# Optimization experiments

Hardware: AMD Instinct MI355X
Metric: run time of the kernel (lower is better)

The kernel has to match this reference:

```python
import jax, jax.numpy as jnp
import numpy as np
from math import sqrt

B, S, E, H = 4, 2048, 1024, 16
D = E // H  # per-head dim = 64


def setup_inputs() -> dict:
    key = jax.random.key(0)
    ks = jax.random.split(key, 11)
    f = lambda k, shape, scale=1.0: jax.random.normal(k, shape, dtype=jnp.float32) * scale
    return {
        "Q": f(ks[0], (B, S, E)),
        "K": f(ks[1], (B, S, E)),
        "V": f(ks[2], (B, S, E)),
        "Wq": f(ks[3], (E, E), 1.0 / sqrt(E)),
        "bq": f(ks[4], (E,), 0.02),
        "Wk": f(ks[5], (E, E), 1.0 / sqrt(E)),
        "bk": f(ks[6], (E,), 0.02),
        "Wv": f(ks[7], (E, E), 1.0 / sqrt(E)),
        "bv": f(ks[8], (E,), 0.02),
        "Wo": f(ks[9], (E, E), 1.0 / sqrt(E)),
        "bo": f(ks[10], (E,), 0.02),
    }


def reference(Q, K, V, Wq, bq, Wk, bk, Wv, bv, Wo, bo):
    # Linear projections (torch Linear: x @ W.T + b)
    q = Q @ Wq.T + bq  # [B,S,E]
    k = K @ Wk.T + bk
    v = V @ Wv.T + bv
    # torch.chunk along last dim into H heads == reshape [B,S,H,D]
    q = q.reshape(B, S, H, D)
    k = k.reshape(B, S, H, D)
    v = v.reshape(B, S, H, D)
    scale = 1.0 / sqrt(D)
    # batched-over-heads scaled dot-product attention
    scores = jnp.einsum("bqhd,bkhd->bhqk", q, k) * scale  # [B,H,S,S]
    attn = jax.nn.softmax(scores, axis=-1)
    out = jnp.einsum("bhqk,bkhd->bqhd", attn, v).reshape(B, S, E)
    # dropout p=0.0 -> identity
    return out @ Wo.T + bo
```

## Files before the change

kernel.cpp:

```cpp
#include <hip/hip_runtime.h>
#include <hip/hip_bf16.h>

#define B_SZ   4
#define S_LEN  2048
#define E_DIM  1024
#define H_NUM  16
#define D_DIM  64
#define M_ROWS (B_SZ * S_LEN)
#define QK_SCALE 0.1803368801111204f

typedef __attribute__((ext_vector_type(8))) __bf16 bf16x8;
typedef __attribute__((ext_vector_type(4))) float  f32x4;

__device__ __forceinline__ bf16x8 load8(const void* p) {
    return __builtin_bit_cast(bf16x8, *reinterpret_cast<const uint4*>(p));
}

#if defined(__has_builtin)
#if __has_builtin(__builtin_amdgcn_exp2f)
#define EXP2F(x) __builtin_amdgcn_exp2f(x)
#endif
#if __has_builtin(__builtin_amdgcn_global_load_lds)
#define HAVE_GLL 1
#endif
#endif
#ifndef EXP2F
#define EXP2F(x) exp2f(x)
#endif

__device__ __forceinline__ void stage16(const __hip_bfloat16* g, __hip_bfloat16* lbase, int lane) {
#ifdef HAVE_GLL
    __builtin_amdgcn_global_load_lds((const __attribute__((address_space(1))) unsigned int*)g,
                                     (__attribute__((address_space(3))) unsigned int*)lbase,
                                     16, 0, 0);
#else
    reinterpret_cast<uint4*>(lbase)[lane] = *reinterpret_cast<const uint4*>(g);
#endif
}

#define N8A (1 << 20)
#define N8W (1 << 17)
#define N8TOT (3 * N8A + 4 * N8W)

struct CvtArgs {
    const float* s[7];
    __hip_bfloat16* d[7];
};

__global__ __launch_bounds__(256) void cvt_all(CvtArgs a)
{
    const int i = blockIdx.x * 256 + threadIdx.x;
    if (i >= N8TOT) return;
    int seg, off;
    if (i < 3 * N8A) { seg = i >> 20;              off = i & (N8A - 1); }
    else             { const int j = i - 3 * N8A;
                       seg = 3 + (j >> 17);        off = j & (N8W - 1); }
    const float* s = a.s[seg];
    __hip_bfloat16* d = a.d[seg];
    const float4 x = reinterpret_cast<const float4*>(s)[off * 2];
    const float4 y = reinterpret_cast<const float4*>(s)[off * 2 + 1];
    __hip_bfloat16 o[8];
    o[0] = __float2bfloat16(x.x); o[1] = __float2bfloat16(x.y);
    o[2] = __float2bfloat16(x.z); o[3] = __float2bfloat16(x.w);
    o[4] = __float2bfloat16(y.x); o[5] = __float2bfloat16(y.y);
    o[6] = __float2bfloat16(y.z); o[7] = __float2bfloat16(y.w);
    reinterpret_cast<uint4*>(d)[off] = *reinterpret_cast<uint4*>(o);
}

__global__ __launch_bounds__(256) void cvt_f32_bf16(const float* __restrict__ s,
                                                    __hip_bfloat16* __restrict__ d,
                                                    int n8)
{
    const int i = blockIdx.x * 256 + threadIdx.x;
    if (i >= n8) return;
    const float4 a = reinterpret_cast<const float4*>(s)[i * 2];
    const float4 b = reinterpret_cast<const float4*>(s)[i * 2 + 1];
    __hip_bfloat16 o[8];
    o[0] = __float2bfloat16(a.x); o[1] = __float2bfloat16(a.y);
    o[2] = __float2bfloat16(a.z); o[3] = __float2bfloat16(a.w);
    o[4] = __float2bfloat16(b.x); o[5] = __float2bfloat16(b.y);
    o[6] = __float2bfloat16(b.z); o[7] = __float2bfloat16(b.w);
    reinterpret_cast<uint4*>(d)[i] = *reinterpret_cast<uint4*>(o);
}

struct GemmArgs {
    const __hip_bfloat16* A[3];
    const __hip_bfloat16* W[3];
    const float* bias[3];
    void* C[3];
    float scale[3];
    int mode[3];
};

__global__ __launch_bounds__(512, 4) void gemm_bt(GemmArgs g)
{
    __shared__ __attribute__((aligned(16))) char lds_raw[3 * 24576];

    const int tid = threadIdx.x;
    const int wid = tid >> 6, lane = tid & 63;
    const int quad = lane >> 4, l16 = lane & 15;
    const int wm = wid >> 2, wn = wid & 3;

    const int seg = blockIdx.x >> 8;
    int bid = blockIdx.x & 255;
    bid = (bid & 7) * 32 + (bid >> 3);
    const int bm = bid >> 2, bn = bid & 3;
    const int row0 = bm * 128, col0 = bn * 256;

    const __hip_bfloat16* A = g.A[seg];
    const __hip_bfloat16* W = g.W[seg];

    const int s_line = tid >> 3, s_gr = tid & 7;
    const int glin  = s_gr ^ (s_line & 7);
    const int s_row = (s_line << 1) + (glin >> 2);
    const int s_ks  = glin & 3;
    const __hip_bfloat16* gA = A + (size_t)(row0 + s_row) * E_DIM + s_ks * 8;
    const __hip_bfloat16* gB = W + (size_t)(col0 + s_row) * E_DIM + s_ks * 8;
    const int stA = wid << 10;

    const int rg   = (((l16 & 1) << 2) | quad) ^ ((l16 >> 1) & 7);
    const int aoff = (wm * 32 + (l16 >> 1)) * 128 + rg * 16;
    const int boff = (wn * 32 + (l16 >> 1)) * 128 + rg * 16;

    f32x4 acc[4][4];
    const f32x4 zero = {0.f, 0.f, 0.f, 0.f};
#pragma unroll
    for (int i = 0; i < 4; i++)
#pragma unroll
        for (int j = 0; j < 4; j++) acc[i][j] = zero;

    auto stage_t = [&](int t) {
        char* b = lds_raw + (t % 3) * 24576;
        const int ko = t * 32;
        stage16(gA + ko, (__hip_bfloat16*)(b + stA), lane);
        stage16(gB + ko, (__hip_bfloat16*)(b + 8192 + stA), lane);
        stage16(gB + (size_t)128 * E_DIM + ko, (__hip_bfloat16*)(b + 16384 + stA), lane);
    };

    auto body = [&](int t, bool stg) {
        __builtin_amdgcn_s_barrier();
        __builtin_amdgcn_sched_barrier(0);
        if (stg) stage_t(t + 2);
        const char* ab = lds_raw + (t % 3) * 24576;
        bf16x8 af[4], bf[4];
#pragma unroll
        for (int i = 0; i < 4; i++) af[i] = load8(ab + aoff + i * 1024);
#pragma unroll
        for (int j = 0; j < 4; j++) bf[j] = load8(ab + 8192 + boff + j * 1024);
        __builtin_amdgcn_s_setprio(1);
#pragma unroll
        for (int i = 0; i < 4; i++)
#pragma unroll
            for (int j = 0; j < 4; j++)
                acc[i][j] = __builtin_amdgcn_mfma_f32_16x16x32_bf16(af[i], bf[j], acc[i][j], 0, 0, 0);
        __builtin_amdgcn_s_setprio(0);
        __builtin_amdgcn_sched_barrier(0);
    };

    const int NT = E_DIM / 32;
    stage_t(0); stage_t(1);
    for (int t = 0; t < NT - 2; ++t) {
        asm volatile("s_waitcnt vmcnt(3)" ::: "memory");
        body(t, true);
    }
    asm volatile("s_waitcnt vmcnt(3)" ::: "memory"); body(NT - 2, false);
    asm volatile("s_waitcnt vmcnt(0)" ::: "memory"); body(NT - 1, false);

    const int   mode  = g.mode[seg];
    const float scale = g.scale[seg];
    const float* bias = g.bias[seg];
    void* Cout        = g.C[seg];
#pragma unroll
    for (int j = 0; j < 4; j++) {
        const int col = col0 + wn * 64 + j * 16 + l16;
        const float bv = bias[col];
#pragma unroll
        for (int i = 0; i < 4; i++) {
            const int row = row0 + wm * 64 + i * 16 + quad * 4;
            if (mode == 3) {
                __attribute__((aligned(8))) __hip_bfloat16 o[4];
#pragma unroll
                for (int r = 0; r < 4; r++) o[r] = __float2bfloat16((acc[i][j][r] + bv) * scale);
                const int b_ = row >> 11, s_ = row & 2047, h_ = col >> 6, d_ = col & 63;
                *reinterpret_cast<uint2*>((__hip_bfloat16*)Cout +
                    (((size_t)(b_ * H_NUM + h_)) << 17) + (d_ << 11) + s_) =
                    *reinterpret_cast<uint2*>(o);
            } else {
#pragma unroll
                for (int r = 0; r < 4; r++) {
                    const float v = (acc[i][j][r] + bv) * scale;
                    const int rr = row + r;
                    if (mode == 0) {
                        ((__hip_bfloat16*)Cout)[(size_t)rr * E_DIM + col] = __float2bfloat16(v);
                    } else if (mode == 1) {
                        ((float*)Cout)[(size_t)rr * E_DIM + col] = v;
                    } else {
                        const int b_ = rr >> 11, s_ = rr & 2047, h_ = col >> 6, d_ = col & 63;
                        ((__hip_bfloat16*)Cout)[(((size_t)(b_ * H_NUM + h_)) << 17) + (s_ << 6) + d_] =
                            __float2bfloat16(v);
                    }
                }
            }
        }
    }
}

__global__ __launch_bounds__(512) void attn(const __hip_bfloat16* __restrict__ Qt,
                                            const __hip_bfloat16* __restrict__ Kt,
                                            const __hip_bfloat16* __restrict__ Vt,
                                            __hip_bfloat16* __restrict__ Op)
{
    __shared__ __hip_bfloat16 Pls[8][64][40];
    __shared__ __attribute__((aligned(16))) __hip_bfloat16 Kls[2][32 * 64];
    __shared__ __attribute__((aligned(16))) __hip_bfloat16 Vls[2][64 * 32];

    const int x = blockIdx.x;
    const int bh     = (x & 7) * 8 + ((x >> 3) & 7);
    const int qchunk = x >> 6;
    const int tid = threadIdx.x;
    const int wave = tid >> 6, lane = tid & 63;
    const int quad = lane >> 4, l16 = lane & 15;
    const int qrow0 = qchunk * 512 + wave * 64;

    const __hip_bfloat16* qb = Qt + ((size_t)bh << 17);
    const __hip_bfloat16* kb = Kt + ((size_t)bh << 17);
    const __hip_bfloat16* vb = Vt + ((size_t)bh << 17);
    __hip_bfloat16* pw = &Pls[wave][0][0];

    const int rt = tid & 255;
    const int skey = rt >> 3, sgk = (rt & 7) ^ (skey & 7);
    const __hip_bfloat16* kSrc = kb + (skey << 6) + (sgk << 3);
    const int sd = rt >> 2, sgv = (rt & 3) ^ ((sd >> 1) & 3);
    const __hip_bfloat16* vSrc = vb + ((size_t)sd << 11) + (sgv << 3);
    const int stW = (wave & 3) << 10;

    const int ksw = l16 & 7, vsw = (l16 >> 1) & 3;

    bf16x8 qf[4][2];
#pragma unroll
    for (int qt = 0; qt < 4; qt++) {
        qf[qt][0] = load8(qb + ((qrow0 + qt * 16 + l16) << 6) + quad * 8);
        qf[qt][1] = load8(qb + ((qrow0 + qt * 16 + l16) << 6) + 32 + quad * 8);
    }

    const f32x4 zero = {0.f, 0.f, 0.f, 0.f};
    f32x4 o_acc[4][4];
#pragma unroll
    for (int qt = 0; qt < 4; qt++)
#pragma unroll
        for (int dj = 0; dj < 4; dj++) o_acc[qt][dj] = zero;
    float lsum[4] = {0.f, 0.f, 0.f, 0.f};

    auto stageKV = [&](int kv, int b) {
        if (tid < 256)
            stage16(kSrc + (kv << 6), (__hip_bfloat16*)((char*)&Kls[b][0] + stW), lane);
        else
            stage16(vSrc + kv,        (__hip_bfloat16*)((char*)&Vls[b][0] + stW), lane);
    };

    auto compute = [&](int b) {
        const char* Kbuf = (const char*)&Kls[b][0];
        const char* Vbuf = (const char*)&Vls[b][0];
#pragma unroll
        for (int t = 0; t < 2; t++) {
            const bf16x8 ka = load8(Kbuf + ((t * 16 + l16) << 7) + ((quad ^ ksw) << 4));
            const bf16x8 kc = load8(Kbuf + ((t * 16 + l16) << 7) + (((quad + 4) ^ ksw) << 4));
#pragma unroll
            for (int qt = 0; qt < 4; qt++) {
                f32x4 st = __builtin_amdgcn_mfma_f32_16x16x32_bf16(ka, qf[qt][0], zero, 0, 0, 0);
                st       = __builtin_amdgcn_mfma_f32_16x16x32_bf16(kc, qf[qt][1], st, 0, 0, 0);
                const float p0 = EXP2F(st[0]), p1 = EXP2F(st[1]);
                const float p2 = EXP2F(st[2]), p3 = EXP2F(st[3]);
                lsum[qt] += (p0 + p1) + (p2 + p3);
                const unsigned u0 = (unsigned)__bfloat16_as_ushort(__float2bfloat16(p0));
                const unsigned u1 = (unsigned)__bfloat16_as_ushort(__float2bfloat16(p1));
                const unsigned u2 = (unsigned)__bfloat16_as_ushort(__float2bfloat16(p2));
                const unsigned u3 = (unsigned)__bfloat16_as_ushort(__float2bfloat16(p3));
                uint2 w;
                w.x = (u1 << 16) | u0;
                w.y = (u3 << 16) | u2;
                *reinterpret_cast<uint2*>(&pw[(qt * 16 + l16) * 40 + t * 16 + quad * 4]) = w;
            }
        }
        bf16x8 vf[4];
#pragma unroll
        for (int dj = 0; dj < 4; dj++)
            vf[dj] = load8(Vbuf + ((dj * 16 + l16) << 6) + ((quad ^ vsw) << 4));
        __builtin_amdgcn_s_setprio(1);
#pragma unroll
        for (int qt = 0; qt < 4; qt++) {
            const bf16x8 pa = load8(&pw[(qt * 16 + l16) * 40 + quad * 8]);
#pragma unroll
            for (int dj = 0; dj < 4; dj++)
                o_acc[qt][dj] = __builtin_amdgcn_mfma_f32_16x16x32_bf16(pa, vf[dj], o_acc[qt][dj], 0, 0, 0);
        }
        __builtin_amdgcn_s_setprio(0);
    };

    stageKV(0, 0);
    int cur = 0;
    for (int kv0 = 0; kv0 < S_LEN; kv0 += 32) {
        __syncthreads();
        if (kv0 + 32 < S_LEN) stageKV(kv0 + 32, cur ^ 1);
        compute(cur);
        cur ^= 1;
    }

    const int b_ = bh >> 4, h_ = bh & 15;
#pragma unroll
    for (int qt = 0; qt < 4; qt++) {
        float l = lsum[qt];
        l += __shfl_xor(l, 16, 64);
        l += __shfl_xor(l, 32, 64);
#pragma unroll
        for (int r = 0; r < 4; r++) {
            const float lr = __shfl(l, quad * 4 + r, 64);
            const float inv = 1.f / lr;
            const size_t ro = ((size_t)b_ * S_LEN + (qrow0 + qt * 16 + quad * 4 + r)) * E_DIM + h_ * D_DIM;
#pragma unroll
            for (int dj = 0; dj < 4; dj++)
                Op[ro + dj * 16 + l16] = __float2bfloat16(o_acc[qt][dj][r] * inv);
        }
    }
}

extern "C" void kernel_launch(void* const* d_in, const int* in_sizes, int n_in,
                              void* d_out, int out_size, void* d_ws, size_t ws_size,
                              hipStream_t stream)
{
    const float* Qf  = (const float*)d_in[0];
    const float* Kf  = (const float*)d_in[1];
    const float* Vf  = (const float*)d_in[2];
    const float* Wqf = (const float*)d_in[3];
    const float* bqf = (const float*)d_in[4];
    const float* Wkf = (const float*)d_in[5];
    const float* bkf = (const float*)d_in[6];
    const float* Wvf = (const float*)d_in[7];
    const float* bvf = (const float*)d_in[8];
    const float* Wof = (const float*)d_in[9];
    const float* bof = (const float*)d_in[10];

    const size_t n_act = (size_t)M_ROWS * E_DIM;
    const size_t n_w   = (size_t)E_DIM * E_DIM;

    const dim3 blk(256), gblk(512), ablk(512);
    const int cg_act = (int)(n_act / 8 / 256);
    const int cg_w   = (int)(n_w / 8 / 256);

    const size_t need_fast = (6 * n_act + 4 * n_w) * sizeof(__hip_bfloat16);

    if (ws_size >= need_fast) {
        __hip_bfloat16* Xq = (__hip_bfloat16*)d_ws;
        __hip_bfloat16* Xk = Xq + n_act;
        __hip_bfloat16* Xv = Xk + n_act;
        __hip_bfloat16* Wb = Xv + n_act;
        __hip_bfloat16* Qt = Wb + 4 * n_w;
        __hip_bfloat16* Kt = Qt + n_act;
        __hip_bfloat16* Vt = Kt + n_act;

        CvtArgs ca;
        ca.s[0] = Qf;  ca.s[1] = Kf;  ca.s[2] = Vf;
        ca.s[3] = Wqf; ca.s[4] = Wkf; ca.s[5] = Wvf; ca.s[6] = Wof;
        ca.d[0] = Xq;  ca.d[1] = Xk;  ca.d[2] = Xv;
        ca.d[3] = Wb;  ca.d[4] = Wb + n_w; ca.d[5] = Wb + 2 * n_w; ca.d[6] = Wb + 3 * n_w;
        cvt_all<<<dim3(N8TOT / 256), blk, 0, stream>>>(ca);

        GemmArgs qkv;
        qkv.A[0] = Xq;  qkv.A[1] = Xk;  qkv.A[2] = Xv;
        qkv.W[0] = Wb;  qkv.W[1] = Wb + n_w;  qkv.W[2] = Wb + 2*n_w;
        qkv.bias[0] = bqf;  qkv.bias[1] = bkf;  qkv.bias[2] = bvf;
        qkv.C[0] = Qt;  qkv.C[1] = Kt;  qkv.C[2] = Vt;
        qkv.scale[0] = QK_SCALE;  qkv.scale[1] = 1.0f;  qkv.scale[2] = 1.0f;
        qkv.mode[0] = 2;  qkv.mode[1] = 2;  qkv.mode[2] = 3;
        gemm_bt<<<dim3(768), gblk, 0, stream>>>(qkv);

        attn<<<dim3(256), ablk, 0, stream>>>(Qt, Kt, Vt, Xq);

        GemmArgs og;
        og.A[0] = Xq;  og.A[1] = Xq;  og.A[2] = Xq;
        og.W[0] = Wb + 3*n_w;  og.W[1] = og.W[0];  og.W[2] = og.W[0];
        og.bias[0] = bof;  og.bias[1] = bof;  og.bias[2] = bof;
        og.C[0] = d_out;  og.C[1] = d_out;  og.C[2] = d_out;
        og.scale[0] = 1.0f;  og.scale[1] = 1.0f;  og.scale[2] = 1.0f;
        og.mode[0] = 1;  og.mode[1] = 1;  og.mode[2] = 1;
        gemm_bt<<<dim3(256), gblk, 0, stream>>>(og);
    } else {
        __hip_bfloat16* X  = (__hip_bfloat16*)d_ws;
        __hip_bfloat16* Wb = X + n_act;
        __hip_bfloat16* Qt = Wb + n_w;
        __hip_bfloat16* Kt = Qt + n_act;
        __hip_bfloat16* Vt = Kt + n_act;

        auto one = [&](const float* Af, const float* Wf, const float* bf_,
                       void* C, float sc, int md) {
            cvt_f32_bf16<<<cg_act, blk, 0, stream>>>(Af, X, (int)(n_act / 8));
            cvt_f32_bf16<<<cg_w,   blk, 0, stream>>>(Wf, Wb, (int)(n_w / 8));
            GemmArgs a;
            a.A[0] = X; a.A[1] = X; a.A[2] = X;
            a.W[0] = Wb; a.W[1] = Wb; a.W[2] = Wb;
            a.bias[0] = bf_; a.bias[1] = bf_; a.bias[2] = bf_;
            a.C[0] = C; a.C[1] = C; a.C[2] = C;
            a.scale[0] = sc; a.scale[1] = sc; a.scale[2] = sc;
            a.mode[0] = md; a.mode[1] = md; a.mode[2] = md;
            gemm_bt<<<dim3(256), gblk, 0, stream>>>(a);
        };
        one(Qf, Wqf, bqf, Qt, QK_SCALE, 2);
        one(Kf, Wkf, bkf, Kt, 1.0f, 2);
        one(Vf, Wvf, bvf, Vt, 1.0f, 3);
        attn<<<dim3(256), ablk, 0, stream>>>(Qt, Kt, Vt, X);
        cvt_f32_bf16<<<cg_w, blk, 0, stream>>>(Wof, Wb, (int)(n_w / 8));
        GemmArgs og;
        og.A[0] = X; og.A[1] = X; og.A[2] = X;
        og.W[0] = Wb; og.W[1] = Wb; og.W[2] = Wb;
        og.bias[0] = bof; og.bias[1] = bof; og.bias[2] = bof;
        og.C[0] = d_out; og.C[1] = d_out; og.C[2] = d_out;
        og.scale[0] = 1.0f; og.scale[1] = 1.0f; og.scale[2] = 1.0f;
        og.mode[0] = 1; og.mode[1] = 1; og.mode[2] = 1;
        gemm_bt<<<dim3(256), gblk, 0, stream>>>(og);
    }
}
```

Before: 326.1 us.

## Split attention KV range across wave halves and reduce partials in LDS

Each block now covers 256 query rows instead of 512. Its two groups of four waves each process half of the key/value sequence with separate double-buffered LDS tiles, and the grid grows from 256 to 512 blocks. At the end, the partial output accumulators and row sums are combined through a shared-memory buffer, and only the first half writes the output. This is a split-K scheme within a block, meant to raise block count and occupancy on the 256-CU part. In exchange it adds LDS use, a 32-step reduction with a barrier on each step, and doubles Q fragment loads per query row across blocks.

New measurement: 368.1 us. +12.9%, slower.

```diff
diff --git a/kernel.cpp b/kernel.cpp
--- a/kernel.cpp
+++ b/kernel.cpp
@@ -211,8 +211,9 @@
                                             __hip_bfloat16* __restrict__ Op)
 {
     __shared__ __hip_bfloat16 Pls[8][64][40];
-    __shared__ __attribute__((aligned(16))) __hip_bfloat16 Kls[2][32 * 64];
-    __shared__ __attribute__((aligned(16))) __hip_bfloat16 Vls[2][64 * 32];
+    __shared__ __attribute__((aligned(16))) __hip_bfloat16 Kls[2][2][32 * 64];
+    __shared__ __attribute__((aligned(16))) __hip_bfloat16 Vls[2][2][64 * 32];
+    __shared__ __attribute__((aligned(16))) float Mb[1280];
 
     const int x = blockIdx.x;
     const int bh     = (x & 7) * 8 + ((x >> 3) & 7);
@@ -220,7 +221,9 @@
     const int tid = threadIdx.x;
     const int wave = tid >> 6, lane = tid & 63;
     const int quad = lane >> 4, l16 = lane & 15;
-    const int qrow0 = qchunk * 512 + wave * 64;
+    const int rw = wave & 3, kshalf = wave >> 2;
+    const int qrow0 = qchunk * 256 + rw * 64;
+    const int kvbase = kshalf << 10;
 
     const __hip_bfloat16* qb = Qt + ((size_t)bh << 17);
     const __hip_bfloat16* kb = Kt + ((size_t)bh << 17);
@@ -229,10 +232,10 @@
 
     const int rt = tid & 255;
     const int skey = rt >> 3, sgk = (rt & 7) ^ (skey & 7);
-    const __hip_bfloat16* kSrc = kb + (skey << 6) + (sgk << 3);
+    const __hip_bfloat16* kSrc = kb + ((kvbase + skey) << 6) + (sgk << 3);
     const int sd = rt >> 2, sgv = (rt & 3) ^ ((sd >> 1) & 3);
-    const __hip_bfloat16* vSrc = vb + ((size_t)sd << 11) + (sgv << 3);
-    const int stW = (wave & 3) << 10;
+    const __hip_bfloat16* vSrc = vb + ((size_t)sd << 11) + (sgv << 3) + kvbase;
+    const int stW = rw << 10;
 
     const int ksw = l16 & 7, vsw = (l16 >> 1) & 3;
 
@@ -252,15 +255,13 @@
     float lsum[4] = {0.f, 0.f, 0.f, 0.f};
 
     auto stageKV = [&](int kv, int b) {
-        if (tid < 256)
-            stage16(kSrc + (kv << 6), (__hip_bfloat16*)((char*)&Kls[b][0] + stW), lane);
-        else
-            stage16(vSrc + kv,        (__hip_bfloat16*)((char*)&Vls[b][0] + stW), lane);
+        stage16(kSrc + (kv << 6), (__hip_bfloat16*)((char*)&Kls[kshalf][b][0] + stW), lane);
+        stage16(vSrc + kv,        (__hip_bfloat16*)((char*)&Vls[kshalf][b][0] + stW), lane);
     };
 
     auto compute = [&](int b) {
-        const char* Kbuf = (const char*)&Kls[b][0];
-        const char* Vbuf = (const char*)&Vls[b][0];
+        const char* Kbuf = (const char*)&Kls[kshalf][b][0];
+        const char* Vbuf = (const char*)&Vls[kshalf][b][0];
 #pragma unroll
         for (int t = 0; t < 2; t++) {
             const bf16x8 ka = load8(Kbuf + ((t * 16 + l16) << 7) + ((quad ^ ksw) << 4));
@@ -299,12 +300,31 @@
 
     stageKV(0, 0);
     int cur = 0;
-    for (int kv0 = 0; kv0 < S_LEN; kv0 += 32) {
+    for (int kv0 = 0; kv0 < 1024; kv0 += 32) {
         __syncthreads();
-        if (kv0 + 32 < S_LEN) stageKV(kv0 + 32, cur ^ 1);
+        if (kv0 + 32 < 1024) stageKV(kv0 + 32, cur ^ 1);
         compute(cur);
         cur ^= 1;
     }
+
+#pragma unroll
+    for (int qt = 0; qt < 4; qt++) {
+#pragma unroll
+        for (int dj = 0; dj < 4; dj++) {
+            if (kshalf == 1) {
+                *reinterpret_cast<f32x4*>(&Mb[(rw * 64 + lane) * 4]) = o_acc[qt][dj];
+                if (dj == 0) Mb[1024 + rw * 64 + lane] = lsum[qt];
+            }
+            __syncthreads();
+            if (kshalf == 0) {
+                const f32x4 v = *reinterpret_cast<const f32x4*>(&Mb[(rw * 64 + lane) * 4]);
+                o_acc[qt][dj] += v;
+                if (dj == 0) lsum[qt] += Mb[1024 + rw * 64 + lane];
+            }
+            __syncthreads();
+        }
+    }
+    if (kshalf == 1) return;
 
     const int b_ = bh >> 4, h_ = bh & 15;
 #pragma unroll
@@ -374,7 +394,7 @@
         qkv.mode[0] = 2;  qkv.mode[1] = 2;  qkv.mode[2] = 3;
         gemm_bt<<<dim3(768), gblk, 0, stream>>>(qkv);
 
-        attn<<<dim3(256), ablk, 0, stream>>>(Qt, Kt, Vt, Xq);
+        attn<<<dim3(512), ablk, 0, stream>>>(Qt, Kt, Vt, Xq);
 
         GemmArgs og;
         og.A[0] = Xq;  og.A[1] = Xq;  og.A[2] = Xq;
@@ -407,7 +427,7 @@
         one(Qf, Wqf, bqf, Qt, QK_SCALE, 2);
         one(Kf, Wkf, bkf, Kt, 1.0f, 2);
         one(Vf, Wvf, bvf, Vt, 1.0f, 3);
-        attn<<<dim3(256), ablk, 0, stream>>>(Qt, Kt, Vt, X);
+        attn<<<dim3(512), ablk, 0, stream>>>(Qt, Kt, Vt, X);
         cvt_f32_bf16<<<cg_w, blk, 0, stream>>>(Wof, Wb, (int)(n_w / 8));
         GemmArgs og;
         og.A[0] = X; og.A[1] = X; og.A[2] = X;
```
